# Optimization experiments

Hardware: AMD Instinct MI355X
Metric: run time of the kernel (lower is better)

Reference implementation:

```python
import jax, jax.numpy as jnp
import numpy as np


def _batched_histc(x, bins):
    # x: [N, ...] -> per-sample histogram over [0, 1], matching torch.histc semantics:
    # bin = floor(v * bins), v == 1.0 goes to last bin, values outside [0,1] ignored.
    N = x.shape[0]
    flat = x.reshape(N, -1)
    idx = jnp.clip((flat * bins).astype(jnp.int32), 0, bins - 1)  # [N, P]
    valid = ((flat >= 0.0) & (flat <= 1.0)).astype(x.dtype)
    gidx = (jnp.arange(N, dtype=jnp.int32)[:, None] * bins + idx).reshape(-1)
    counts = jax.ops.segment_sum(valid.reshape(-1), gidx, num_segments=N * bins)
    return counts.reshape(N, bins)


def _mlp(h, W1, b1, W2, b2, W3, b3, W4, b4):
    h = jax.nn.relu(h @ W1 + b1)
    h = jax.nn.relu(h @ W2 + b2)
    h = jax.nn.relu(h @ W3 + b3)
    return h @ W4 + b4  # [N, 1]


def setup_inputs() -> dict:
    key = jax.random.key(0)
    ks = jax.random.split(key, 5)
    bins = 128
    N, C, H, W = 128, 1, 1024, 1024
    x = jax.random.uniform(ks[0], (N, C, H, W), dtype=jnp.float32)
    def lin(k, fan_in, fan_out):
        s = 1.0 / np.sqrt(fan_in)
        return jax.random.uniform(k, (fan_in, fan_out), jnp.float32, -s, s)
    return {
        "x": x,
        "W1": lin(ks[1], bins, 32), "b1": jnp.zeros((32,), jnp.float32),
        "W2": lin(ks[2], 32, 64),   "b2": jnp.zeros((64,), jnp.float32),
        "W3": lin(ks[3], 64, 128),  "b3": jnp.zeros((128,), jnp.float32),
        "W4": lin(ks[4], 128, 1),   "b4": jnp.zeros((1,), jnp.float32),
        "bins": bins,
    }


def reference(x, W1, b1, W2, b2, W3, b3, W4, b4, bins):
    hst = _batched_histc(x, bins)                       # [N, bins]
    w = _mlp(hst, W1, b1, W2, b2, W3, b3, W4, b4)       # [N, 1]
    w = w[:, :, None, None]                             # [N, 1, 1, 1]
    return x * w
```

## Files before the change

kernel.cpp:

```cpp
#include <hip/hip_runtime.h>

#define N_IMG 128
#define BINS 128
#define HW_ELEMS (1 << 20)
#define CHUNKS 16

__global__ __launch_bounds__(256) void hist_kernel(const float* __restrict__ x,
                                                   int* __restrict__ hist) {
    __shared__ int lh[4][BINS];
    const int tid  = threadIdx.x;
    const int wave = tid >> 6;

    for (int i = tid; i < 4 * BINS; i += 256) ((int*)lh)[i] = 0;
    __syncthreads();

    const int blk   = blockIdx.x;
    const int img   = blk / CHUNKS;
    const int chunk = blk % CHUNKS;
    const int chunk_elems = HW_ELEMS / CHUNKS;
    const long long base = (long long)img * HW_ELEMS + (long long)chunk * chunk_elems;
    const float4* xv = (const float4*)(x + base);
    const int n4 = chunk_elems / 4;

    for (int i = tid; i < n4; i += 256) {
        float4 v = xv[i];
        float vals[4] = {v.x, v.y, v.z, v.w};
        #pragma unroll
        for (int k = 0; k < 4; ++k) {
            float f = vals[k];
            if (f >= 0.0f && f <= 1.0f) {
                int b = (int)(f * (float)BINS);
                b = b > (BINS - 1) ? (BINS - 1) : b;
                atomicAdd(&lh[wave][b], 1);
            }
        }
    }
    __syncthreads();

    for (int b = tid; b < BINS; b += 256) {
        int s = lh[0][b] + lh[1][b] + lh[2][b] + lh[3][b];
        atomicAdd(&hist[img * BINS + b], s);
    }
}

__global__ __launch_bounds__(128) void mlp_kernel(const int* __restrict__ hist,
                                                  const float* __restrict__ W1, const float* __restrict__ b1,
                                                  const float* __restrict__ W2, const float* __restrict__ b2,
                                                  const float* __restrict__ W3, const float* __restrict__ b3,
                                                  const float* __restrict__ W4, const float* __restrict__ b4,
                                                  float* __restrict__ wout) {
    __shared__ float h0[128], a1[32], a2[64], a3[128];
    const int img = blockIdx.x;
    const int t   = threadIdx.x;

    h0[t] = (float)hist[img * BINS + t];
    __syncthreads();

    if (t < 32) {
        float acc = b1[t];
        #pragma unroll 8
        for (int i = 0; i < 128; ++i) acc += h0[i] * W1[i * 32 + t];
        a1[t] = fmaxf(acc, 0.0f);
    }
    __syncthreads();

    if (t < 64) {
        float acc = b2[t];
        #pragma unroll 8
        for (int i = 0; i < 32; ++i) acc += a1[i] * W2[i * 64 + t];
        a2[t] = fmaxf(acc, 0.0f);
    }
    __syncthreads();

    {
        float acc = b3[t];
        #pragma unroll 8
        for (int i = 0; i < 64; ++i) acc += a2[i] * W3[i * 128 + t];
        a3[t] = fmaxf(acc, 0.0f);
    }
    __syncthreads();

    if (t == 0) {
        float acc = b4[0];
        for (int i = 0; i < 128; ++i) acc += a3[i] * W4[i];
        wout[img] = acc;
    }
}

__global__ __launch_bounds__(256) void scale_kernel(const float* __restrict__ x,
                                                    const float* __restrict__ w,
                                                    float* __restrict__ out,
                                                    long long n4) {
    const long long stride = (long long)gridDim.x * blockDim.x;
    const float4* xv = (const float4*)x;
    float4* ov = (float4*)out;
    for (long long i = (long long)blockIdx.x * blockDim.x + threadIdx.x; i < n4; i += stride) {
        int img = (int)(i >> 18);
        float s = w[img];
        float4 v = xv[i];
        v.x *= s; v.y *= s; v.z *= s; v.w *= s;
        ov[i] = v;
    }
}

extern "C" void kernel_launch(void* const* d_in, const int* in_sizes, int n_in,
                              void* d_out, int out_size, void* d_ws, size_t ws_size,
                              hipStream_t stream) {
    const float* x  = (const float*)d_in[0];
    const float* W1 = (const float*)d_in[1];
    const float* b1 = (const float*)d_in[2];
    const float* W2 = (const float*)d_in[3];
    const float* b2 = (const float*)d_in[4];
    const float* W3 = (const float*)d_in[5];
    const float* b3 = (const float*)d_in[6];
    const float* W4 = (const float*)d_in[7];
    const float* b4 = (const float*)d_in[8];

    int*   hist = (int*)d_ws;
    float* wout = (float*)((char*)d_ws + (size_t)N_IMG * BINS * sizeof(int));

    hipMemsetAsync(d_ws, 0, (size_t)N_IMG * BINS * sizeof(int), stream);

    hist_kernel<<<N_IMG * CHUNKS, 256, 0, stream>>>(x, hist);

    mlp_kernel<<<N_IMG, 128, 0, stream>>>(hist, W1, b1, W2, b2, W3, b3, W4, b4, wout);

    const long long n4 = (long long)N_IMG * HW_ELEMS / 4;
    scale_kernel<<<8192, 256, 0, stream>>>(x, wout, (float*)d_out, n4);
}
```

Baseline: 348.6 us.

## Replicate LDS histograms per 16 threads, write partial histograms, nontemporal stores

```diff
diff --git a/kernel.cpp b/kernel.cpp
--- a/kernel.cpp
+++ b/kernel.cpp
@@ -4,14 +4,18 @@
 #define BINS 128
 #define HW_ELEMS (1 << 20)
 #define CHUNKS 16
+#define NCOPY 16
+#define HPAD 132
+
+typedef float f32x4 __attribute__((ext_vector_type(4)));
 
 __global__ __launch_bounds__(256) void hist_kernel(const float* __restrict__ x,
-                                                   int* __restrict__ hist) {
-    __shared__ int lh[4][BINS];
-    const int tid  = threadIdx.x;
-    const int wave = tid >> 6;
+                                                   int* __restrict__ parthist) {
+    __shared__ int lh[NCOPY * HPAD];
+    const int tid = threadIdx.x;
+    const int cpy = tid >> 4;
 
-    for (int i = tid; i < 4 * BINS; i += 256) ((int*)lh)[i] = 0;
+    for (int i = tid; i < NCOPY * HPAD; i += 256) lh[i] = 0;
     __syncthreads();
 
     const int blk   = blockIdx.x;
@@ -19,31 +23,34 @@
     const int chunk = blk % CHUNKS;
     const int chunk_elems = HW_ELEMS / CHUNKS;
     const long long base = (long long)img * HW_ELEMS + (long long)chunk * chunk_elems;
-    const float4* xv = (const float4*)(x + base);
+    const f32x4* xv = (const f32x4*)(x + base);
     const int n4 = chunk_elems / 4;
 
+    int* myh = &lh[cpy * HPAD];
+
     for (int i = tid; i < n4; i += 256) {
-        float4 v = xv[i];
-        float vals[4] = {v.x, v.y, v.z, v.w};
+        f32x4 v = xv[i];
         #pragma unroll
         for (int k = 0; k < 4; ++k) {
-            float f = vals[k];
+            float f = v[k];
             if (f >= 0.0f && f <= 1.0f) {
                 int b = (int)(f * (float)BINS);
                 b = b > (BINS - 1) ? (BINS - 1) : b;
-                atomicAdd(&lh[wave][b], 1);
+                atomicAdd(&myh[b], 1);
             }
         }
     }
     __syncthreads();
 
-    for (int b = tid; b < BINS; b += 256) {
-        int s = lh[0][b] + lh[1][b] + lh[2][b] + lh[3][b];
-        atomicAdd(&hist[img * BINS + b], s);
+    if (tid < BINS) {
+        int s = 0;
+        #pragma unroll
+        for (int c = 0; c < NCOPY; ++c) s += lh[c * HPAD + tid];
+        parthist[blk * BINS + tid] = s;
     }
 }
 
-__global__ __launch_bounds__(128) void mlp_kernel(const int* __restrict__ hist,
+__global__ __launch_bounds__(128) void mlp_kernel(const int* __restrict__ parthist,
                                                   const float* __restrict__ W1, const float* __restrict__ b1,
                                                   const float* __restrict__ W2, const float* __restrict__ b2,
                                                   const float* __restrict__ W3, const float* __restrict__ b3,
@@ -53,7 +60,13 @@
     const int img = blockIdx.x;
     const int t   = threadIdx.x;
 
-    h0[t] = (float)hist[img * BINS + t];
+    {
+        int s = 0;
+        #pragma unroll
+        for (int c = 0; c < CHUNKS; ++c)
+            s += parthist[(img * CHUNKS + c) * BINS + t];
+        h0[t] = (float)s;
+    }
     __syncthreads();
 
     if (t < 32) {
@@ -92,14 +105,14 @@
                                                     float* __restrict__ out,
                                                     long long n4) {
     const long long stride = (long long)gridDim.x * blockDim.x;
-    const float4* xv = (const float4*)x;
-    float4* ov = (float4*)out;
+    const f32x4* xv = (const f32x4*)x;
+    f32x4* ov = (f32x4*)out;
     for (long long i = (long long)blockIdx.x * blockDim.x + threadIdx.x; i < n4; i += stride) {
         int img = (int)(i >> 18);
         float s = w[img];
-        float4 v = xv[i];
-        v.x *= s; v.y *= s; v.z *= s; v.w *= s;
-        ov[i] = v;
+        f32x4 v = xv[i];
+        v *= s;
+        __builtin_nontemporal_store(v, &ov[i]);
     }
 }
 
@@ -116,14 +129,12 @@
     const float* W4 = (const float*)d_in[7];
     const float* b4 = (const float*)d_in[8];
 
-    int*   hist = (int*)d_ws;
-    float* wout = (float*)((char*)d_ws + (size_t)N_IMG * BINS * sizeof(int));
+    int*   parthist = (int*)d_ws;
+    float* wout = (float*)((char*)d_ws + (size_t)N_IMG * CHUNKS * BINS * sizeof(int));
 
-    hipMemsetAsync(d_ws, 0, (size_t)N_IMG * BINS * sizeof(int), stream);
+    hist_kernel<<<N_IMG * CHUNKS, 256, 0, stream>>>(x, parthist);
 
-    hist_kernel<<<N_IMG * CHUNKS, 256, 0, stream>>>(x, hist);
-
-    mlp_kernel<<<N_IMG, 128, 0, stream>>>(hist, W1, b1, W2, b2, W3, b3, W4, b4, wout);
+    mlp_kernel<<<N_IMG, 128, 0, stream>>>(parthist, W1, b1, W2, b2, W3, b3, W4, b4, wout);
 
     const long long n4 = (long long)N_IMG * HW_ELEMS / 4;
     scale_kernel<<<8192, 256, 0, stream>>>(x, wout, (float*)d_out, n4);
```

Result: faster. 311.3 us (-10.7%).
